# Kernel tuning notes

Measured on AMD Instinct MI355X. Metric: run time of the kernel, lower is better.

## Reference

```python
import jax, jax.numpy as jnp
from jax import lax
import numpy as np

HEADS = 8
SR = 4  # sr_ratio
LN_EPS = 1e-5


def gaussian_filt(x, kernel_size, sigma):
    # depthwise gaussian blur, x: [B, C, H, W]
    ch = x.shape[1]
    c = jnp.arange(kernel_size, dtype=x.dtype)
    xx = jnp.broadcast_to(c[None, :], (kernel_size, kernel_size))
    yy = xx.T
    mean = (kernel_size - 1) / 2.0
    g = jnp.exp(-((xx - mean) ** 2 + (yy - mean) ** 2) / (2.0 * sigma * sigma))
    g = g / g.sum()  # normalization cancels the 1/(2*pi*var) factor
    kern = jnp.broadcast_to(g[None, None], (ch, 1, kernel_size, kernel_size)).astype(x.dtype)
    p = (kernel_size - 1) // 2
    return lax.conv_general_dilated(
        x, kern, (1, 1), [(p, p), (p, p)],
        dimension_numbers=('NCHW', 'OIHW', 'NCHW'), feature_group_count=ch)


def reconstruct_feature(feature, mask, kernel_size, sigma):
    if kernel_size <= 1:
        return feature
    feature = feature * mask
    out = gaussian_filt(jnp.concatenate([feature, mask], axis=1), kernel_size, sigma)
    f_int = out[:, :-1]
    m_int = out[:, -1:]
    f_int = f_int / (m_int + 1e-6)
    m_bin = (m_int > 0).astype(feature.dtype)
    f_int = f_int * m_bin
    return feature + (1.0 - mask) * f_int


def token2map(x, loc, H, W, kernel_size, sigma):
    # x: [B, N, C], loc: [B, N, 2] in [0,1]
    B, N, C = x.shape
    loc = jnp.clip(loc, 0.0, 1.0) * jnp.array([W - 1, H - 1], dtype=loc.dtype)
    loc = jnp.round(loc).astype(jnp.int32)
    idx = loc[..., 0] + loc[..., 1] * W + (jnp.arange(B, dtype=jnp.int32) * (H * W))[:, None]
    src = jnp.concatenate([x, jnp.ones((B, N, 1), x.dtype)], axis=-1).reshape(B * N, C + 1)
    out = jax.ops.segment_sum(src, idx.reshape(-1), num_segments=B * H * W)
    out = out.reshape(B, H, W, C + 1).transpose(0, 3, 1, 2)  # [B, C+1, H, W]
    feature, mask = out[:, :-1], out[:, -1:]
    feature = feature / (mask + 1e-6)
    mask = (mask > 0).astype(x.dtype)
    feature = feature * mask
    return reconstruct_feature(feature, mask, kernel_size, sigma)


def layer_norm(x, w, b):
    mu = jnp.mean(x, axis=-1, keepdims=True)
    var = jnp.mean((x - mu) ** 2, axis=-1, keepdims=True)
    return (x - mu) * lax.rsqrt(var + LN_EPS) * w + b


def forward(x, x_source, loc_source, conf_source, Wq, Wk, Wv, sr_w, sr_b, ln_w, ln_b, Wp, bp, H, W):
    B, N, C = x.shape
    dh = C // HEADS
    scale = dh ** -0.5
    q = (x @ Wq.T).reshape(B, N, HEADS, dh).transpose(0, 2, 1, 3)  # [B,h,N,dh]
    # token2map + spatial reduction
    xm = token2map(x_source, loc_source, H, W, SR - 1, 2.0)        # [B,C,H,W]
    xs = lax.conv_general_dilated(
        xm, sr_w, (SR, SR), 'VALID',
        dimension_numbers=('NCHW', 'OIHW', 'NCHW')) + sr_b[None, :, None, None]
    xs = xs.reshape(B, C, -1).transpose(0, 2, 1)                   # [B,Ns,C]
    xs = layer_norm(xs, ln_w, ln_b)
    Ns = xs.shape[1]
    k = (xs @ Wk.T).reshape(B, Ns, HEADS, dh).transpose(0, 2, 1, 3)
    v = (xs @ Wv.T).reshape(B, Ns, HEADS, dh).transpose(0, 2, 1, 3)
    attn = jnp.einsum('bhnd,bhmd->bhnm', q, k) * scale             # [B,h,N,Ns]
    attn = attn + conf_source[..., 0][:, None, None, :]            # additive bias
    attn = jax.nn.softmax(attn, axis=-1)
    out = jnp.einsum('bhnm,bhmd->bhnd', attn, v)
    out = out.transpose(0, 2, 1, 3).reshape(B, N, C)
    return out @ Wp.T + bp


def setup_inputs() -> dict:
    key = jax.random.key(0)
    ks = jax.random.split(key, 10)
    B, N, C, Hm = 2, 8192, 256, 128
    Ns = (Hm // SR) * (Hm // SR)
    s = 0.02
    return {
        'x': jax.random.normal(ks[0], (B, N, C), jnp.float32),
        'x_source': jax.random.normal(ks[1], (B, N, C), jnp.float32),
        'loc_source': jax.random.uniform(ks[2], (B, N, 2), jnp.float32),
        'conf_source': jax.random.normal(ks[3], (B, Ns, 1), jnp.float32),
        'Wq': jax.random.normal(ks[4], (C, C), jnp.float32) * s,
        'Wk': jax.random.normal(ks[5], (C, C), jnp.float32) * s,
        'Wv': jax.random.normal(ks[6], (C, C), jnp.float32) * s,
        'sr_w': jax.random.normal(ks[7], (C, C, SR, SR), jnp.float32) * s,
        'sr_b': jnp.zeros((C,), jnp.float32),
        'ln_w': jnp.ones((C,), jnp.float32),
        'ln_b': jnp.zeros((C,), jnp.float32),
        'Wp': jax.random.normal(ks[8], (C, C), jnp.float32) * s,
        'bp': jnp.zeros((C,), jnp.float32),
        'H': Hm,
        'W': Hm,
    }


def reference(x, x_source, loc_source, conf_source, Wq, Wk, Wv, sr_w, sr_b, ln_w, ln_b, Wp, bp, H, W):
    return forward(x, x_source, loc_source, conf_source, Wq, Wk, Wv, sr_w, sr_b, ln_w, ln_b, Wp, bp, H, W)
```

## Files before the change

### kernel.cpp

```cpp
#include <hip/hip_runtime.h>
#include <hip/hip_bf16.h>
#include <cstddef>
#include <cstdint>

#define NTOK 8192
#define CD   256
#define HWPIX 16384
#define WIDTH 128
#define NSEQ 1024

typedef __attribute__((ext_vector_type(8))) short bfrag;
typedef __attribute__((ext_vector_type(4))) float f32x4;
typedef __attribute__((ext_vector_type(4))) unsigned int u32x4;

__device__ inline unsigned short f2bfu(float f) {
    __hip_bfloat16 h = __float2bfloat16(f);
    unsigned short u;
    __builtin_memcpy(&u, &h, 2);
    return u;
}
__device__ inline unsigned int rtn16(float f) {
    unsigned int u = __builtin_bit_cast(unsigned int, f);
    return u + 0x7fffu + ((u >> 16) & 1u);
}
__device__ inline float bits2f(unsigned int u) {
    return __builtin_bit_cast(float, u);
}
__device__ inline void gld16(const unsigned short* g, const unsigned short* l) {
    __builtin_amdgcn_global_load_lds(
        (const __attribute__((address_space(1))) unsigned int*)g,
        (__attribute__((address_space(3))) unsigned int*)l, 16, 0, 0);
}
__device__ inline unsigned int cvtpk(float lo, float hi) {
    unsigned int r;
    asm("v_cvt_pk_bf16_f32 %0, %1, %2" : "=v"(r) : "v"(lo), "v"(hi));
    return r;
}
__device__ inline int kslot(int rin) {
    return (((rin >> 5) * 2 + ((rin >> 2) & 1)) << 4)
         + (((rin >> 3) & 3) << 2) + (rin & 3);
}

__global__ __launch_bounds__(256) void scatter_prep(
        const float* __restrict__ xsrc, const float* __restrict__ loc,
        float* __restrict__ feat, float* __restrict__ maskr,
        const float* __restrict__ srw, const float* __restrict__ Wq,
        const float* __restrict__ Wk, const float* __restrict__ Wv,
        const float* __restrict__ Wp, const float* __restrict__ conf,
        const float* __restrict__ x,
        unsigned short* __restrict__ wTb, unsigned short* __restrict__ wqb,
        unsigned short* __restrict__ wkb, unsigned short* __restrict__ wvb,
        unsigned short* __restrict__ wpb, unsigned short* __restrict__ stg,
        unsigned short* __restrict__ xbf) {
    int gid = blockIdx.x, tid = threadIdx.x;
    if (gid < 16384) {
        int token = gid;
        int b = token >> 13;
        float lx = loc[token * 2 + 0];
        float ly = loc[token * 2 + 1];
        lx = fminf(fmaxf(lx, 0.f), 1.f) * 127.0f;
        ly = fminf(fmaxf(ly, 0.f), 1.f) * 127.0f;
        int ix = __float2int_rn(lx);
        int iy = __float2int_rn(ly);
        int p = b * HWPIX + iy * WIDTH + ix;
        atomicAdd(&feat[(size_t)p * CD + tid], xsrc[(size_t)token * CD + tid]);
        if (tid == 0) atomicAdd(&maskr[p], 1.0f);
    } else if (gid < 20480) {
        int idx = (gid - 16384) * 256 + tid;
        int co = idx >> 12;
        int rest = idx & 4095;
        int k16 = rest >> 8;
        int ci = rest & 255;
        int kh = k16 >> 2, kw = k16 & 3;
        wTb[idx] = f2bfu(srw[(size_t)co * 4096 + ci * 16 + kh * 4 + kw]);
    } else if (gid < 20672) {
        const float* s; unsigned short* d; int base;
        if (gid < 20544)      { s = Wq; d = wqb; base = gid - 20480; }
        else if (gid < 20608) { s = Wk; d = wkb; base = gid - 20544; }
        else                  { s = Wv; d = wvb; base = gid - 20608; }
        int i = (base * 256 + tid) * 4;
        float4 v = *(const float4*)(s + i);
        ushort4 o;
        o.x = f2bfu(v.x); o.y = f2bfu(v.y); o.z = f2bfu(v.z); o.w = f2bfu(v.w);
        *(ushort4*)(d + i) = o;
    } else if (gid < 20928) {
        int n = gid - 20672, t = tid;
        float w = Wp[n * 256 + t];
        unsigned short hu = f2bfu(w);
        float hf = bits2f(((unsigned int)hu) << 16);
        unsigned short lu = f2bfu(w - hf);
        wpb[n * 768 + t]       = hu;
        wpb[n * 768 + 256 + t] = lu;
        wpb[n * 768 + 512 + t] = hu;
    } else if (gid < 20936) {
        int idx = (gid - 20928) * 256 + tid;
        int b = idx >> 10, key = idx & 1023;
        int tile = key >> 6, rin = key & 63;
        int slot = kslot(rin);
        float val = conf[idx] * 1.4426950408889634f;
        #pragma unroll
        for (int h = 0; h < 8; h++)
            *(float*)&stg[((size_t)((b * 8 + h) * 16 + tile)) * 5120
                          + 4864 + slot * 2] = val;
    } else {
        size_t idx = ((size_t)(gid - 20936) * 256 + tid) * 4;
        float4 v = *(const float4*)(x + idx);
        ushort4 o;
        o.x = f2bfu(v.x); o.y = f2bfu(v.y); o.z = f2bfu(v.z); o.w = f2bfu(v.w);
        *(ushort4*)(xbf + idx) = o;
    }
}

__global__ __launch_bounds__(256) void recon_patch(const float* __restrict__ feat,
        const float* __restrict__ maskr, unsigned short* __restrict__ apatch) {
    __shared__ float s_wci[36];
    __shared__ float s_vb[36];
    __shared__ int   s_np[36];
    __shared__ float s_ginv[16];
    __shared__ float s_omb[16];
    int blk = blockIdx.x;
    int b  = blk >> 10;
    int py = (blk >> 5) & 31;
    int px = blk & 31;
    int c = threadIdx.x;
    const float e1 = 0.882496902584595f;
    const float e2 = 0.778800783071405f;
    const float snorm = 1.0f / (1.0f + 4.0f * e1 + 4.0f * e2);
    int y0 = py * 4 - 1, x0 = px * 4 - 1;
    if (c < 36) {
        int ry = c / 6, rx = c % 6;
        int yy = y0 + ry, xx = x0 + rx;
        bool valid = (yy >= 0 && yy <= 127 && xx >= 0 && xx <= 127);
        int yc = min(max(yy, 0), 127), xc = min(max(xx, 0), 127);
        int np_ = b * HWPIX + yc * WIDTH + xc;
        float m = maskr[np_];
        float bin = (m > 0.f) ? 1.f : 0.f;
        float inv = 1.0f / (m + 1e-6f);
        s_wci[c] = valid ? bin * inv : 0.f;
        s_vb[c]  = valid ? bin : 0.f;
        s_np[c]  = np_;
    }
    __syncthreads();
    if (c < 16) {
        int oy = c >> 2, ox = c & 3;
        float gm = 0.f;
        #pragma unroll
        for (int dy = -1; dy <= 1; dy++)
            #pragma unroll
            for (int dx = -1; dx <= 1; dx++) {
                int manh = (dy != 0) + (dx != 0);
                float g = ((manh == 2) ? e2 : (manh == 1) ? e1 : 1.0f) * snorm;
                gm += g * s_vb[(oy + 1 + dy) * 6 + (ox + 1 + dx)];
            }
        s_ginv[c] = (gm > 0.f) ? 1.0f / (gm + 1e-6f) : 0.f;
        s_omb[c]  = 1.0f - s_vb[(oy + 1) * 6 + (ox + 1)];
    }
    float gf[4][4], fcv[4][4];
    #pragma unroll
    for (int oy = 0; oy < 4; oy++)
        #pragma unroll
        for (int ox = 0; ox < 4; ox++) { gf[oy][ox] = 0.f; fcv[oy][ox] = 0.f; }
    #pragma unroll
    for (int ry = 0; ry < 6; ry++) {
        #pragma unroll
        for (int rx = 0; rx < 6; rx++) {
            int j = ry * 6 + rx;
            float f = feat[(size_t)s_np[j] * CD + c] * s_wci[j];
            #pragma unroll
            for (int oy = 0; oy < 4; oy++) {
                int dy = ry - 1 - oy;
                if (dy < -1 || dy > 1) continue;
                #pragma unroll
                for (int ox = 0; ox < 4; ox++) {
                    int dx = rx - 1 - ox;
                    if (dx < -1 || dx > 1) continue;
                    int manh = (dy != 0) + (dx != 0);
                    float g = ((manh == 2) ? e2 : (manh == 1) ? e1 : 1.0f) * snorm;
                    gf[oy][ox] += g * f;
                }
            }
            if (ry >= 1 && ry <= 4 && rx >= 1 && rx <= 4)
                fcv[ry - 1][rx - 1] = f;
        }
    }
    __syncthreads();
    int r = b * 1024 + py * 32 + px;
    size_t base = (size_t)r * 4096 + c;
    #pragma unroll
    for (int oy = 0; oy < 4; oy++)
        #pragma unroll
        for (int ox = 0; ox < 4; ox++) {
            int i = oy * 4 + ox;
            float f_int = gf[oy][ox] * s_ginv[i];
            float res = fcv[oy][ox] + s_omb[i] * f_int;
            apatch[base + (size_t)i * 256] = f2bfu(res);
        }
}

__device__ __forceinline__ void bgemm_body(
        unsigned short* As, unsigned short* Bs,
        const unsigned short* __restrict__ A,
        const unsigned short* __restrict__ B, const float* __restrict__ bias,
        float* __restrict__ C, unsigned short* __restrict__ dstb,
        int M, int N, int K, int kSplit, int mode, float mult,
        int bx, int by, int bz) {
    int tid = threadIdx.x;
    int wave = tid >> 6, lane = tid & 63, m15 = lane & 15, quad = lane >> 4;
    int wr = (wave >> 1) * 64, wc = (wave & 1) * 64;
    int m0 = by * 128, n0 = bx * 128;
    int kchunk = K / kSplit, k0 = bz * kchunk;
    int srow = tid >> 2, sko = (tid & 3) * 8;
    f32x4 acc[4][4];
    #pragma unroll
    for (int i = 0; i < 4; i++)
        #pragma unroll
        for (int j = 0; j < 4; j++) acc[i][j] = (f32x4){0.f, 0.f, 0.f, 0.f};
    const unsigned short* Ag = A + (size_t)(m0 + srow) * K + k0 + sko;
    const unsigned short* Bg = B + (size_t)(n0 + srow) * K + k0 + sko;
    for (int kk = 0; kk < kchunk; kk += 32) {
        bfrag a0 = *(const bfrag*)(Ag + kk);
        bfrag a1 = *(const bfrag*)(Ag + (size_t)64 * K + kk);
        bfrag b0 = *(const bfrag*)(Bg + kk);
        bfrag b1 = *(const bfrag*)(Bg + (size_t)64 * K + kk);
        __syncthreads();
        *(bfrag*)&As[srow * 32 + sko] = a0;
        *(bfrag*)&As[(srow + 64) * 32 + sko] = a1;
        *(bfrag*)&Bs[srow * 32 + sko] = b0;
        *(bfrag*)&Bs[(srow + 64) * 32 + sko] = b1;
        __syncthreads();
        bfrag af[4], bfr[4];
        #pragma unroll
        for (int mi = 0; mi < 4; mi++)
            af[mi] = *(const bfrag*)&As[(wr + mi * 16 + m15) * 32 + quad * 8];
        #pragma unroll
        for (int ni = 0; ni < 4; ni++)
            bfr[ni] = *(const bfrag*)&Bs[(wc + ni * 16 + m15) * 32 + quad * 8];
        #pragma unroll
        for (int mi = 0; mi < 4; mi++)
            #pragma unroll
            for (int ni = 0; ni < 4; ni++)
                acc[mi][ni] = __builtin_amdgcn_mfma_f32_16x16x32_bf16(
                                  af[mi], bfr[ni], acc[mi][ni], 0, 0, 0);
    }
    if (mode == 2) {
        #pragma unroll
        for (int mi = 0; mi < 4; mi++) {
            #pragma unroll
            for (int i = 0; i < 4; i++) {
                int row = m0 + wr + mi * 16 + quad * 4 + i;
                int b = row >> 13, r = row & 8191;
                #pragma unroll
                for (int ni = 0; ni < 4; ni++) {
                    int col = n0 + wc + ni * 16 + m15;
                    int h = col >> 5, d = col & 31;
                    size_t di = ((((size_t)(b * 8 + h)) << 13) + r) * 32 + d;
                    dstb[di] = f2bfu(acc[mi][ni][i] * mult);
                }
            }
        }
    } else if (mode == 3) {
        #pragma unroll
        for (int mi = 0; mi < 4; mi++) {
            #pragma unroll
            for (int i = 0; i < 4; i++) {
                int row = m0 + wr + mi * 16 + quad * 4 + i;
                int b = row >> 10, key = row & 1023;
                int tile = key >> 6, rin = key & 63;
                int slot = kslot(rin);
                #pragma unroll
                for (int ni = 0; ni < 4; ni++) {
                    int col = n0 + wc + ni * 16 + m15;
                    unsigned short v = f2bfu(acc[mi][ni][i]);
                    if (col < 256) {
                        int h = col >> 5, d = col & 31;
                        size_t di = ((size_t)((b * 8 + h) * 16 + tile)) * 5120
                                    + slot * 40 + d;
                        dstb[di] = v;
                    } else {
                        int c2 = col - 256;
                        int h = c2 >> 5, d = c2 & 31;
                        size_t di = ((size_t)((b * 8 + h) * 16 + tile)) * 5120
                                    + 2560 + d * 72 + rin;
                        dstb[di] = v;
                    }
                }
            }
        }
    } else if (mode == 4) {
        #pragma unroll
        for (int mi = 0; mi < 4; mi++) {
            #pragma unroll
            for (int i = 0; i < 4; i++) {
                size_t row = ((size_t)bz * M + m0 + wr + mi * 16 + quad * 4 + i) * N;
                #pragma unroll
                for (int ni = 0; ni < 4; ni++) {
                    int col = n0 + wc + ni * 16 + m15;
                    C[row + col] = acc[mi][ni][i];
                }
            }
        }
    } else {
        #pragma unroll
        for (int mi = 0; mi < 4; mi++) {
            #pragma unroll
            for (int i = 0; i < 4; i++) {
                size_t row = (size_t)(m0 + wr + mi * 16 + quad * 4 + i) * N;
                #pragma unroll
                for (int ni = 0; ni < 4; ni++) {
                    int col = n0 + wc + ni * 16 + m15;
                    C[row + col] = acc[mi][ni][i] + (bias ? bias[col] : 0.f);
                }
            }
        }
    }
}

__global__ __launch_bounds__(256) void bgemm(const unsigned short* A,
        const unsigned short* B, const float* bias,
        float* C, unsigned short* dstb,
        int M, int N, int K, int kSplit, int mode, float mult) {
    __shared__ __align__(16) unsigned short As[128 * 32];
    __shared__ __align__(16) unsigned short Bs[128 * 32];
    bgemm_body(As, Bs, A, B, bias, C, dstb, M, N, K, kSplit, mode, mult,
               blockIdx.x, blockIdx.y, blockIdx.z);
}

__global__ __launch_bounds__(256) void qkv_fused(const unsigned short* xbf,
        const unsigned short* wqb, const unsigned short* xsbf,
        const unsigned short* wkb, unsigned short* Qbf,
        unsigned short* stg, float SC) {
    __shared__ __align__(16) unsigned short As[128 * 32];
    __shared__ __align__(16) unsigned short Bs[128 * 32];
    int g = blockIdx.x;
    if (g < 256) {
        bgemm_body(As, Bs, xbf, wqb, nullptr, nullptr, Qbf,
                   16384, 256, 256, 1, 2, SC, g & 1, g >> 1, 0);
    } else {
        int g2 = g - 256;
        bgemm_body(As, Bs, xsbf, wkb, nullptr, nullptr, stg,
                   2048, 512, 256, 1, 3, 1.f, g2 & 3, g2 >> 2, 0);
    }
}

__global__ __launch_bounds__(256) void ln_red(const float* __restrict__ part,
        const float* __restrict__ srb, const float* __restrict__ w,
        const float* __restrict__ bvec, unsigned short* __restrict__ outb) {
    int row = blockIdx.x;
    int c = threadIdx.x;
    float v = srb[c];
    #pragma unroll
    for (int z = 0; z < 8; z++)
        v += part[((size_t)z * 2048 + row) * 256 + c];
    __shared__ float red[4];
    float s = v;
    #pragma unroll
    for (int o = 32; o >= 1; o >>= 1) s += __shfl_down(s, o, 64);
    if ((c & 63) == 0) red[c >> 6] = s;
    __syncthreads();
    float mean = (red[0] + red[1] + red[2] + red[3]) * (1.f / 256.f);
    __syncthreads();
    float d = v - mean;
    float s2 = d * d;
    #pragma unroll
    for (int o = 32; o >= 1; o >>= 1) s2 += __shfl_down(s2, o, 64);
    if ((c & 63) == 0) red[c >> 6] = s2;
    __syncthreads();
    float var = (red[0] + red[1] + red[2] + red[3]) * (1.f / 256.f);
    float r = 1.0f / sqrtf(var + 1e-5f);
    outb[(size_t)row * 256 + c] = f2bfu(d * r * w[c] + bvec[c]);
}

__global__ __launch_bounds__(256, 4) void attn_v11(
        const unsigned short* __restrict__ Qb,
        const unsigned short* __restrict__ STG,
        unsigned short* __restrict__ aout) {
    __shared__ __align__(16) unsigned short SB[3][5120];
    int tid  = threadIdx.x;
    int wave = tid >> 6;
    int lane = tid & 63;
    int m15  = lane & 15;
    int quad = lane >> 4;
    int flat = blockIdx.y * 64 + blockIdx.x;
    int j  = flat >> 3;
    int bh = (flat & 7) + ((j >> 6) << 3);
    int b  = bh >> 3;
    int h  = bh & 7;
    int qbase = (j & 63) * 128 + wave * 32;

    const unsigned short* qp = Qb + ((size_t)bh * NTOK + qbase) * 32;
    bfrag Qa0 = *(const bfrag*)(qp + m15 * 32 + quad * 8);
    bfrag Qa1 = *(const bfrag*)(qp + (16 + m15) * 32 + quad * 8);
    const unsigned short* sg = STG + (size_t)bh * 16 * 5120;

    bfrag ones;
    #pragma unroll
    for (int i = 0; i < 8; i++) ones[i] = (short)0x3F80;

    f32x4 O[2][2];
    f32x4 Lac[2];
    #pragma unroll
    for (int tq = 0; tq < 2; tq++) {
        O[tq][0] = (f32x4){0.f, 0.f, 0.f, 0.f};
        O[tq][1] = (f32x4){0.f, 0.f, 0.f, 0.f};
        Lac[tq]  = (f32x4){0.f, 0.f, 0.f, 0.f};
    }

    #pragma unroll
    for (int pt = 0; pt < 2; pt++) {
        const unsigned short* g = sg + (size_t)pt * 5120;
        unsigned short* l = &SB[pt][0];
        gld16(g + wave * 512 + lane * 8, l + wave * 512);
        gld16(g + (wave + 4) * 512 + lane * 8, l + (wave + 4) * 512);
        if (wave < 2) gld16(g + (8 + wave) * 512 + lane * 8, l + (8 + wave) * 512);
    }

    int cur = 0;
    for (int t = 0; t < 16; t++) {
        if (t < 15) {
            if (wave < 2) asm volatile("s_waitcnt vmcnt(3)" ::: "memory");
            else          asm volatile("s_waitcnt vmcnt(2)" ::: "memory");
        } else {
            asm volatile("s_waitcnt vmcnt(0)" ::: "memory");
        }
        __builtin_amdgcn_s_barrier();
        __builtin_amdgcn_sched_barrier(0);
        const unsigned short* Ks = &SB[0][0] + cur * 5120;
        const unsigned short* Vs = Ks + 2560;
        const float* Cf = (const float*)(Ks + 4864);
        bfrag kf[4]; f32x4 ccf[4];
        #pragma unroll
        for (int s = 0; s < 4; s++) {
            kf[s]  = *(const bfrag*)&Ks[(s * 16 + m15) * 40 + quad * 8];
            ccf[s] = *(const f32x4*)&Cf[s * 16 + quad * 4];
        }
        if (t < 14) {
            int nxt = cur + 2; if (nxt >= 3) nxt -= 3;
            const unsigned short* g = sg + (size_t)(t + 2) * 5120;
            unsigned short* l = &SB[0][0] + nxt * 5120;
            gld16(g + wave * 512 + lane * 8, l + wave * 512);
            gld16(g + (wave + 4) * 512 + lane * 8, l + (wave + 4) * 512);
            if (wave < 2) gld16(g + (8 + wave) * 512 + lane * 8,
                                l + (8 + wave) * 512);
        }
        f32x4 S[2][4];
        __builtin_amdgcn_s_setprio(1);
        #pragma unroll
        for (int s = 0; s < 4; s++) {
            S[0][s] = __builtin_amdgcn_mfma_f32_16x16x32_bf16(kf[s], Qa0,
                                                              ccf[s], 0, 0, 0);
            S[1][s] = __builtin_amdgcn_mfma_f32_16x16x32_bf16(kf[s], Qa1,
                                                              ccf[s], 0, 0, 0);
        }
        __builtin_amdgcn_s_setprio(0);
        bfrag Pb[2][2];
        #pragma unroll
        for (int tq = 0; tq < 2; tq++) {
            float v[4][4];
            #pragma unroll
            for (int s = 0; s < 4; s++)
                #pragma unroll
                for (int r = 0; r < 4; r++)
                    v[s][r] = __builtin_amdgcn_exp2f(S[tq][s][r]);
            #pragma unroll
            for (int k2 = 0; k2 < 2; k2++) {
                u32x4 pw;
                pw[0] = cvtpk(v[2 * k2][0],     v[2 * k2][1]);
                pw[1] = cvtpk(v[2 * k2][2],     v[2 * k2][3]);
                pw[2] = cvtpk(v[2 * k2 + 1][0], v[2 * k2 + 1][1]);
                pw[3] = cvtpk(v[2 * k2 + 1][2], v[2 * k2 + 1][3]);
                Pb[tq][k2] = __builtin_bit_cast(bfrag, pw);
            }
        }
        bfrag vfr[2][2];
        #pragma unroll
        for (int k2 = 0; k2 < 2; k2++)
            #pragma unroll
            for (int dt = 0; dt < 2; dt++)
                vfr[k2][dt] = *(const bfrag*)&Vs[(dt * 16 + m15) * 72 +
                                                 k2 * 32 + quad * 8];
        __builtin_amdgcn_s_setprio(1);
        #pragma unroll
        for (int k2 = 0; k2 < 2; k2++)
            #pragma unroll
            for (int tq = 0; tq < 2; tq++) {
                #pragma unroll
                for (int dt = 0; dt < 2; dt++)
                    O[tq][dt] = __builtin_amdgcn_mfma_f32_16x16x32_bf16(
                                    Pb[tq][k2], vfr[k2][dt], O[tq][dt], 0, 0, 0);
                Lac[tq] = __builtin_amdgcn_mfma_f32_16x16x32_bf16(
                                    Pb[tq][k2], ones, Lac[tq], 0, 0, 0);
            }
        __builtin_amdgcn_s_setprio(0);
        cur = (cur == 2) ? 0 : cur + 1;
    }
    #pragma unroll
    for (int tq = 0; tq < 2; tq++) {
        #pragma unroll
        for (int r = 0; r < 4; r++) {
            float inv = 1.0f / Lac[tq][r];
            int row = b * NTOK + qbase + tq * 16 + quad * 4 + r;
            size_t rb = (size_t)row * 768;
            #pragma unroll
            for (int dt = 0; dt < 2; dt++) {
                float o = O[tq][dt][r] * inv;
                unsigned int hr = rtn16(o);
                unsigned short hu = hr >> 16;
                float hf = bits2f(hr & 0xffff0000u);
                unsigned short lu = rtn16(o - hf) >> 16;
                int col = h * 32 + dt * 16 + m15;
                aout[rb + col]       = hu;
                aout[rb + 256 + col] = hu;
                aout[rb + 512 + col] = lu;
            }
        }
    }
}

extern "C" void kernel_launch(void* const* d_in, const int* in_sizes, int n_in,
                              void* d_out, int out_size, void* d_ws, size_t ws_size,
                              hipStream_t stream) {
    const float* x        = (const float*)d_in[0];
    const float* x_source = (const float*)d_in[1];
    const float* loc      = (const float*)d_in[2];
    const float* conf     = (const float*)d_in[3];
    const float* Wq       = (const float*)d_in[4];
    const float* Wk       = (const float*)d_in[5];
    const float* Wv       = (const float*)d_in[6];
    const float* srw      = (const float*)d_in[7];
    const float* srb      = (const float*)d_in[8];
    const float* lnw      = (const float*)d_in[9];
    const float* lnb      = (const float*)d_in[10];
    const float* Wp       = (const float*)d_in[11];
    const float* bp       = (const float*)d_in[12];
    float* out = (float*)d_out;
    float* ws  = (float*)d_ws;

    float* feat = ws;
    unsigned short* Qbf = (unsigned short*)ws;
    float* maskr = ws + 8388608;
    unsigned short* apatch = (unsigned short*)(ws + 8421376);
    unsigned short* aouts  = (unsigned short*)(ws + 8421376);
    unsigned short* wTb    = (unsigned short*)(ws + 12615680);
    unsigned short* stg  = (unsigned short*)(ws + 14712832);
    unsigned short* wqb  = (unsigned short*)(ws + 15368192);
    unsigned short* wkb  = (unsigned short*)(ws + 15400960);
    unsigned short* wvb  = (unsigned short*)(ws + 15433728);
    unsigned short* wpb  = (unsigned short*)(ws + 15466496);
    unsigned short* xsbf = (unsigned short*)(ws + 16089088);
    unsigned short* xbf  = (unsigned short*)(ws + 16351232);
    float*          part = ws + 18448384;

    const float SC = 0.17677669529663687f * 1.4426950408889634f;

    hipMemsetAsync(feat, 0, (size_t)(8388608 + 32768) * sizeof(float), stream);

    scatter_prep<<<25032, 256, 0, stream>>>(x_source, loc, feat, maskr,
                                            srw, Wq, Wk, Wv, Wp, conf, x,
                                            wTb, wqb, wkb, wvb, wpb, stg, xbf);
    recon_patch<<<2048, 256, 0, stream>>>(feat, maskr, apatch);
    bgemm<<<dim3(2, 16, 8), 256, 0, stream>>>(apatch, wTb, nullptr,
                                              part, nullptr,
                                              2048, 256, 4096, 8, 4, 1.f);
    ln_red<<<2048, 256, 0, stream>>>(part, srb, lnw, lnb, xsbf);
    qkv_fused<<<320, 256, 0, stream>>>(xbf, wqb, xsbf, wkb, Qbf, stg, SC);
    attn_v11<<<dim3(64, 16), 256, 0, stream>>>(Qbf, stg, aouts);
    bgemm<<<dim3(2, 128, 1), 256, 0, stream>>>(aouts, wpb, bp,
                                               out, nullptr,
                                               16384, 256, 768, 1, 0, 1.f);
}
```

Measured before the change: 232.0 us.

## Halve GEMM M-tile and fold duplicated attention-output columns in projection

Templates the bf16 GEMM on M-tile size and uses 64-row tiles for the SR conv GEMM, QKV GEMM and output projection, doubling block counts for better occupancy and load balance. The attention output no longer stores the duplicated high-bf16 half. The projection GEMM instead remaps its K index with a fold offset, reading the same columns twice. This reduces attention write traffic and workspace size, at the cost of less per-block data reuse with smaller tiles.

```diff
diff --git a/kernel.cpp b/kernel.cpp
--- a/kernel.cpp
+++ b/kernel.cpp
@@ -197,46 +197,52 @@
         }
 }
 
+template<int TM>
 __device__ __forceinline__ void bgemm_body(
         unsigned short* As, unsigned short* Bs,
         const unsigned short* __restrict__ A,
         const unsigned short* __restrict__ B, const float* __restrict__ bias,
         float* __restrict__ C, unsigned short* __restrict__ dstb,
-        int M, int N, int K, int kSplit, int mode, float mult,
-        int bx, int by, int bz) {
+        int M, int N, int K, int Ka, int kfold, int kSplit, int mode,
+        float mult, int bx, int by, int bz) {
+    constexpr int WRH = TM / 2;
+    constexpr int MI  = WRH / 16;
     int tid = threadIdx.x;
     int wave = tid >> 6, lane = tid & 63, m15 = lane & 15, quad = lane >> 4;
-    int wr = (wave >> 1) * 64, wc = (wave & 1) * 64;
-    int m0 = by * 128, n0 = bx * 128;
+    int wr = (wave >> 1) * WRH, wc = (wave & 1) * 64;
+    int m0 = by * TM, n0 = bx * 128;
     int kchunk = K / kSplit, k0 = bz * kchunk;
     int srow = tid >> 2, sko = (tid & 3) * 8;
-    f32x4 acc[4][4];
-    #pragma unroll
-    for (int i = 0; i < 4; i++)
+    f32x4 acc[MI][4];
+    #pragma unroll
+    for (int i = 0; i < MI; i++)
         #pragma unroll
         for (int j = 0; j < 4; j++) acc[i][j] = (f32x4){0.f, 0.f, 0.f, 0.f};
-    const unsigned short* Ag = A + (size_t)(m0 + srow) * K + k0 + sko;
+    const unsigned short* Ag = A + (size_t)(m0 + srow) * Ka + sko;
     const unsigned short* Bg = B + (size_t)(n0 + srow) * K + k0 + sko;
     for (int kk = 0; kk < kchunk; kk += 32) {
-        bfrag a0 = *(const bfrag*)(Ag + kk);
-        bfrag a1 = *(const bfrag*)(Ag + (size_t)64 * K + kk);
+        int kl = k0 + kk;
+        int ke = (kfold && kl >= kfold) ? kl - kfold : kl;
+        bfrag a0 = *(const bfrag*)(Ag + ke);
+        bfrag a1;
+        if constexpr (TM == 128) a1 = *(const bfrag*)(Ag + (size_t)64 * Ka + ke);
         bfrag b0 = *(const bfrag*)(Bg + kk);
         bfrag b1 = *(const bfrag*)(Bg + (size_t)64 * K + kk);
         __syncthreads();
         *(bfrag*)&As[srow * 32 + sko] = a0;
-        *(bfrag*)&As[(srow + 64) * 32 + sko] = a1;
+        if constexpr (TM == 128) *(bfrag*)&As[(srow + 64) * 32 + sko] = a1;
         *(bfrag*)&Bs[srow * 32 + sko] = b0;
         *(bfrag*)&Bs[(srow + 64) * 32 + sko] = b1;
         __syncthreads();
-        bfrag af[4], bfr[4];
-        #pragma unroll
-        for (int mi = 0; mi < 4; mi++)
+        bfrag af[MI], bfr[4];
+        #pragma unroll
+        for (int mi = 0; mi < MI; mi++)
             af[mi] = *(const bfrag*)&As[(wr + mi * 16 + m15) * 32 + quad * 8];
         #pragma unroll
         for (int ni = 0; ni < 4; ni++)
             bfr[ni] = *(const bfrag*)&Bs[(wc + ni * 16 + m15) * 32 + quad * 8];
         #pragma unroll
-        for (int mi = 0; mi < 4; mi++)
+        for (int mi = 0; mi < MI; mi++)
             #pragma unroll
             for (int ni = 0; ni < 4; ni++)
                 acc[mi][ni] = __builtin_amdgcn_mfma_f32_16x16x32_bf16(
@@ -244,7 +250,7 @@
     }
     if (mode == 2) {
         #pragma unroll
-        for (int mi = 0; mi < 4; mi++) {
+        for (int mi = 0; mi < MI; mi++) {
             #pragma unroll
             for (int i = 0; i < 4; i++) {
                 int row = m0 + wr + mi * 16 + quad * 4 + i;
@@ -260,7 +266,7 @@
         }
     } else if (mode == 3) {
         #pragma unroll
-        for (int mi = 0; mi < 4; mi++) {
+        for (int mi = 0; mi < MI; mi++) {
             #pragma unroll
             for (int i = 0; i < 4; i++) {
                 int row = m0 + wr + mi * 16 + quad * 4 + i;
@@ -288,7 +294,7 @@
         }
     } else if (mode == 4) {
         #pragma unroll
-        for (int mi = 0; mi < 4; mi++) {
+        for (int mi = 0; mi < MI; mi++) {
             #pragma unroll
             for (int i = 0; i < 4; i++) {
                 size_t row = ((size_t)bz * M + m0 + wr + mi * 16 + quad * 4 + i) * N;
@@ -301,7 +307,7 @@
         }
     } else {
         #pragma unroll
-        for (int mi = 0; mi < 4; mi++) {
+        for (int mi = 0; mi < MI; mi++) {
             #pragma unroll
             for (int i = 0; i < 4; i++) {
                 size_t row = (size_t)(m0 + wr + mi * 16 + quad * 4 + i) * N;
@@ -315,14 +321,16 @@
     }
 }
 
+template<int TM>
 __global__ __launch_bounds__(256) void bgemm(const unsigned short* A,
         const unsigned short* B, const float* bias,
         float* C, unsigned short* dstb,
-        int M, int N, int K, int kSplit, int mode, float mult) {
+        int M, int N, int K, int Ka, int kfold, int kSplit, int mode,
+        float mult) {
     __shared__ __align__(16) unsigned short As[128 * 32];
     __shared__ __align__(16) unsigned short Bs[128 * 32];
-    bgemm_body(As, Bs, A, B, bias, C, dstb, M, N, K, kSplit, mode, mult,
-               blockIdx.x, blockIdx.y, blockIdx.z);
+    bgemm_body<TM>(As, Bs, A, B, bias, C, dstb, M, N, K, Ka, kfold, kSplit,
+                   mode, mult, blockIdx.x, blockIdx.y, blockIdx.z);
 }
 
 __global__ __launch_bounds__(256) void qkv_fused(const unsigned short* xbf,
@@ -332,13 +340,13 @@
     __shared__ __align__(16) unsigned short As[128 * 32];
     __shared__ __align__(16) unsigned short Bs[128 * 32];
     int g = blockIdx.x;
-    if (g < 256) {
-        bgemm_body(As, Bs, xbf, wqb, nullptr, nullptr, Qbf,
-                   16384, 256, 256, 1, 2, SC, g & 1, g >> 1, 0);
+    if (g < 512) {
+        bgemm_body<64>(As, Bs, xbf, wqb, nullptr, nullptr, Qbf,
+                       16384, 256, 256, 256, 0, 1, 2, SC, g & 1, g >> 1, 0);
     } else {
-        int g2 = g - 256;
-        bgemm_body(As, Bs, xsbf, wkb, nullptr, nullptr, stg,
-                   2048, 512, 256, 1, 3, 1.f, g2 & 3, g2 >> 2, 0);
+        int g2 = g - 512;
+        bgemm_body<64>(As, Bs, xsbf, wkb, nullptr, nullptr, stg,
+                       2048, 512, 256, 256, 0, 1, 3, 1.f, g2 & 3, g2 >> 2, 0);
     }
 }
 
@@ -370,7 +378,7 @@
     outb[(size_t)row * 256 + c] = f2bfu(d * r * w[c] + bvec[c]);
 }
 
-__global__ __launch_bounds__(256, 4) void attn_v11(
+__global__ __launch_bounds__(256, 4) void attn_v12(
         const unsigned short* __restrict__ Qb,
         const unsigned short* __restrict__ STG,
         unsigned short* __restrict__ aout) {
@@ -499,7 +507,7 @@
         for (int r = 0; r < 4; r++) {
             float inv = 1.0f / Lac[tq][r];
             int row = b * NTOK + qbase + tq * 16 + quad * 4 + r;
-            size_t rb = (size_t)row * 768;
+            size_t rb = (size_t)row * 512;
             #pragma unroll
             for (int dt = 0; dt < 2; dt++) {
                 float o = O[tq][dt][r] * inv;
@@ -509,8 +517,7 @@
                 unsigned short lu = rtn16(o - hf) >> 16;
                 int col = h * 32 + dt * 16 + m15;
                 aout[rb + col]       = hu;
-                aout[rb + 256 + col] = hu;
-                aout[rb + 512 + col] = lu;
+                aout[rb + 256 + col] = lu;
             }
         }
     }
@@ -558,13 +565,15 @@
                                             srw, Wq, Wk, Wv, Wp, conf, x,
                                             wTb, wqb, wkb, wvb, wpb, stg, xbf);
     recon_patch<<<2048, 256, 0, stream>>>(feat, maskr, apatch);
-    bgemm<<<dim3(2, 16, 8), 256, 0, stream>>>(apatch, wTb, nullptr,
-                                              part, nullptr,
-                                              2048, 256, 4096, 8, 4, 1.f);
+    bgemm<64><<<dim3(2, 32, 8), 256, 0, stream>>>(apatch, wTb, nullptr,
+                                                  part, nullptr,
+                                                  2048, 256, 4096, 4096, 0,
+                                                  8, 4, 1.f);
     ln_red<<<2048, 256, 0, stream>>>(part, srb, lnw, lnb, xsbf);
-    qkv_fused<<<320, 256, 0, stream>>>(xbf, wqb, xsbf, wkb, Qbf, stg, SC);
-    attn_v11<<<dim3(64, 16), 256, 0, stream>>>(Qbf, stg, aouts);
-    bgemm<<<dim3(2, 128, 1), 256, 0, stream>>>(aouts, wpb, bp,
-                                               out, nullptr,
-                                               16384, 256, 768, 1, 0, 1.f);
-}
+    qkv_fused<<<640, 256, 0, stream>>>(xbf, wqb, xsbf, wkb, Qbf, stg, SC);
+    attn_v12<<<dim3(64, 16), 256, 0, stream>>>(Qbf, stg, aouts);
+    bgemm<64><<<dim3(2, 256, 1), 256, 0, stream>>>(aouts, wpb, bp,
+                                                   out, nullptr,
+                                                   16384, 256, 768, 512, 256,
+                                                   1, 0, 1.f);
+}
```

After: 220.7 us. 4.9% less time.
